# Kernel tuning notes

Measured on AMD Instinct MI355X. Metric: run time of the kernel, lower is better.

The kernel has to match this reference:

```python
import jax, jax.numpy as jnp
import numpy as np


def setup_inputs() -> dict:
    key = jax.random.key(0)
    k1, k2, k3, k4 = jax.random.split(key, 4)
    B, C, H, W = 8, 512, 64, 64  # h must equal w per the broadcast in the original
    opt = jax.random.normal(k1, (B, C, H, W), dtype=jnp.float32)
    sar = jax.random.normal(k2, (B, C, H, W), dtype=jnp.float32)
    # 1x1 conv weights, shape [out_c, in_c] (kernel spatial dims are 1x1)
    W_opt = jax.random.normal(k3, (C, C), dtype=jnp.float32) * (2.0 / C) ** 0.5
    W_sar = jax.random.normal(k4, (C, C), dtype=jnp.float32) * (2.0 / C) ** 0.5
    return {"opt": opt, "sar": sar, "W_opt": W_opt, "W_sar": W_sar}


def _branch(x, Wc):
    # 1x1 conv: per-pixel channel mixing. Q = K = V (same conv applied to same input).
    f = jnp.einsum('oc,bchw->bohw', Wc, x)            # (b,c,h,w)
    # S[b,c,i,j] = sum_h Q[b,c,h,i] * K[b,c,h,j]  (transpose(2,3) @ original)
    S = jnp.einsum('bchi,bchj->bcij', f, f)           # (b,c,w,w)
    # nn.Softmax() with no dim on 4D -> softmax over channel dim (axis=1)
    S = jax.nn.softmax(S, axis=1)
    return f, S


def reference(opt, sar, W_opt, W_sar):
    V_opt, S_opt = _branch(opt, W_opt)
    V_sar, S_sar = _branch(sar, W_sar)
    hadamard = S_opt * S_sar                          # (b,c,w,w); h==w lets it broadcast with V
    Att = (V_opt * hadamard) * (V_sar * hadamard)
    return Att
```

## Files before the change

### kernel.cpp

```cpp
#include <hip/hip_runtime.h>
#include <cstdint>

#define CCH 512
#define HW  4096
#define WDIM 64
#define NBATCH 8
#define CHW ((size_t)CCH * HW)

typedef __attribute__((ext_vector_type(8))) short bf16x8;
typedef __attribute__((ext_vector_type(4))) float f32x4;
typedef __attribute__((ext_vector_type(4))) unsigned u32x4;

__device__ __forceinline__ unsigned short f2bf(float x) {
  unsigned u = __float_as_uint(x);
  unsigned r = (u + 0x7FFFu + ((u >> 16) & 1u)) >> 16;
  return (unsigned short)r;
}
__device__ __forceinline__ float bf2f(unsigned short h) {
  return __uint_as_float(((unsigned)h) << 16);
}

__device__ __forceinline__ void gl_lds16(const void* g, void* l) {
  __builtin_amdgcn_global_load_lds(
      (const __attribute__((address_space(1))) void*)g,
      (__attribute__((address_space(3))) void*)l, 16, 0, 0);
}

__global__ __launch_bounds__(256) void wsplit_k(
    const float* __restrict__ Wo, const float* __restrict__ Wsr,
    unsigned short* __restrict__ Whl) {
  const int br = blockIdx.y;
  const float* W = br ? Wsr : Wo;
  const int i = blockIdx.x * 256 + threadIdx.x;
  const float x = W[i];
  const unsigned short h = f2bf(x);
  unsigned short* dst = Whl + (size_t)br * 524288;
  dst[i] = h;
  dst[262144 + i] = f2bf(x - bf2f(h));
}

__global__ __launch_bounds__(256, 2) void mfma_conv_k(
    const unsigned short* __restrict__ Whl,
    const float* __restrict__ opt, const float* __restrict__ sar,
    float* __restrict__ F, int b0) {
  const int z = blockIdx.z;
  const int br = z & 1, bl = z >> 1;
  const unsigned short* Ah_g = Whl + (size_t)br * 524288;
  const unsigned short* Al_g = Ah_g + 262144;
  const float* Xb = (br ? sar : opt) + (size_t)(b0 + bl) * CHW;
  const int n0 = blockIdx.x * 128, m0 = blockIdx.y * 128;

  __shared__ __align__(16) unsigned short Ahs[2][128 * 32];
  __shared__ __align__(16) unsigned short Als[2][128 * 32];
  __shared__ __align__(16) unsigned short Xhs[2][128 * 32];
  __shared__ __align__(16) unsigned short Xls[2][128 * 32];

  const int tid = threadIdx.x;
  const int wave = tid >> 6, lane = tid & 63;
  const int wm = (wave >> 1) * 64, wn = (wave & 1) * 64;

  f32x4 acc[4][4] = {};

  const int rl = lane >> 2;
  const int kcA = (((lane & 3) ^ ((lane >> 3) & 3)) * 8);

  const int rX = lane;
  const int pX = (wave ^ ((lane >> 1) & 3)) * 8;

  const int fr = lane & 15;
  const int kq = (((lane >> 4) ^ ((lane >> 1) & 3)) * 8);

  float xv[16];

  auto stageA = [&](int k0, int cb) {
#pragma unroll
    for (int q = 0; q < 2; ++q) {
      const int rbase = wave * 32 + q * 16;
      const int r = rbase + rl;
      gl_lds16(Ah_g + (size_t)(m0 + r) * CCH + k0 + kcA, &Ahs[cb][rbase * 32]);
      gl_lds16(Al_g + (size_t)(m0 + r) * CCH + k0 + kcA, &Als[cb][rbase * 32]);
    }
  };

  auto loadX = [&](int k0) {
#pragma unroll
    for (int s = 0; s < 8; ++s) {
      const size_t rowb = (size_t)(k0 + wave * 8 + s) * HW + n0;
      xv[s] = Xb[rowb + rX];
      xv[8 + s] = Xb[rowb + 64 + rX];
    }
  };

  auto writeX = [&](int cb) {
    u32x4 h0, h1, l0, l1;
#pragma unroll
    for (int w = 0; w < 4; ++w) {
      const unsigned a0 = __float_as_uint(xv[2 * w]);
      const unsigned a1 = __float_as_uint(xv[2 * w + 1]);
      const unsigned b0_ = __float_as_uint(xv[8 + 2 * w]);
      const unsigned b1_ = __float_as_uint(xv[8 + 2 * w + 1]);
      h0[w] = __builtin_amdgcn_perm(a1, a0, 0x07060302u);
      h1[w] = __builtin_amdgcn_perm(b1_, b0_, 0x07060302u);
      const float la0 = xv[2 * w] - __uint_as_float(a0 & 0xFFFF0000u);
      const float la1 = xv[2 * w + 1] - __uint_as_float(a1 & 0xFFFF0000u);
      const float lb0 = xv[8 + 2 * w] - __uint_as_float(b0_ & 0xFFFF0000u);
      const float lb1 = xv[8 + 2 * w + 1] - __uint_as_float(b1_ & 0xFFFF0000u);
      l0[w] = __builtin_amdgcn_perm(__float_as_uint(la1), __float_as_uint(la0),
                                    0x07060302u);
      l1[w] = __builtin_amdgcn_perm(__float_as_uint(lb1), __float_as_uint(lb0),
                                    0x07060302u);
    }
    *(u32x4*)&Xhs[cb][rX * 32 + pX] = h0;
    *(u32x4*)&Xhs[cb][(rX + 64) * 32 + pX] = h1;
    *(u32x4*)&Xls[cb][rX * 32 + pX] = l0;
    *(u32x4*)&Xls[cb][(rX + 64) * 32 + pX] = l1;
  };

  auto compute = [&](int cb) {
    bf16x8 bh[4], blo[4];
#pragma unroll
    for (int j = 0; j < 4; ++j) {
      const int n = wn + j * 16 + fr;
      bh[j] = *(const bf16x8*)&Xhs[cb][n * 32 + kq];
      blo[j] = *(const bf16x8*)&Xls[cb][n * 32 + kq];
    }
#pragma unroll
    for (int i = 0; i < 4; ++i) {
      const int m = wm + i * 16 + fr;
      const bf16x8 ah = *(const bf16x8*)&Ahs[cb][m * 32 + kq];
      const bf16x8 al = *(const bf16x8*)&Als[cb][m * 32 + kq];
#pragma unroll
      for (int j = 0; j < 4; ++j) {
        acc[i][j] = __builtin_amdgcn_mfma_f32_16x16x32_bf16(ah, bh[j], acc[i][j], 0, 0, 0);
        acc[i][j] = __builtin_amdgcn_mfma_f32_16x16x32_bf16(ah, blo[j], acc[i][j], 0, 0, 0);
        acc[i][j] = __builtin_amdgcn_mfma_f32_16x16x32_bf16(al, bh[j], acc[i][j], 0, 0, 0);
      }
    }
  };

  stageA(0, 0);
  loadX(0);
  writeX(0);
  __syncthreads();

  int cur = 0;
  for (int t = 0; t < 15; ++t) {
    const int k0n = (t + 1) * 32;
    stageA(k0n, cur ^ 1);
    loadX(k0n);
    compute(cur);
    writeX(cur ^ 1);
    __syncthreads();
    cur ^= 1;
  }
  compute(cur);

  float* Fb = F + (size_t)z * CHW;
  const int col = lane & 15, rq = (lane >> 4) * 4;
#pragma unroll
  for (int i = 0; i < 4; ++i)
#pragma unroll
    for (int j = 0; j < 4; ++j) {
      const int n = n0 + wn + j * 16 + col;
#pragma unroll
      for (int r = 0; r < 4; ++r) {
        const int m = m0 + wm + i * 16 + rq + r;
        Fb[(size_t)m * HW + n] = acc[i][j][r];
      }
    }
}

#define FT_S 72
__global__ __launch_bounds__(256, 4) void gram_k(
    const float* __restrict__ F, float* __restrict__ S) {
  const size_t base = ((size_t)blockIdx.y * CCH + blockIdx.x) * HW;
  const float* Fc = F + base;
  float* Sc = S + base;

  __shared__ float Fs[64 * 64];
  __shared__ unsigned short FtH[64 * FT_S];
  __shared__ unsigned short FtL[64 * FT_S];

  const int tid = threadIdx.x;
  const int wave = tid >> 6, lane = tid & 63;

#pragma unroll
  for (int t = 0; t < 4; ++t) {
    const int off = (wave * 4 + t) * 256;
    gl_lds16(Fc + off + lane * 4, &Fs[off]);
  }
  __syncthreads();

  {
    const int w = lane;
    const int hc = wave * 16;
    unsigned short hb[16], lb[16];
#pragma unroll
    for (int k = 0; k < 16; ++k) {
      const float x = Fs[(hc + k) * 64 + w];
      const unsigned short h = f2bf(x);
      hb[k] = h;
      lb[k] = f2bf(x - bf2f(h));
    }
    unsigned short* dh = &FtH[w * FT_S + hc];
    unsigned short* dl = &FtL[w * FT_S + hc];
    *(uint4*)(dh + 0) = *(uint4*)&hb[0];
    *(uint4*)(dh + 8) = *(uint4*)&hb[8];
    *(uint4*)(dl + 0) = *(uint4*)&lb[0];
    *(uint4*)(dl + 8) = *(uint4*)&lb[8];
  }
  __syncthreads();

  const int wm = (wave >> 1) * 32, wn = (wave & 1) * 32;
  const int fr = lane & 15, kq = (lane >> 4) * 8;

  f32x4 acc[2][2] = {};
#pragma unroll
  for (int kcc = 0; kcc < 2; ++kcc) {
    bf16x8 ah[2], al[2], bh[2], bl[2];
#pragma unroll
    for (int i = 0; i < 2; ++i) {
      ah[i] = *(const bf16x8*)&FtH[(wm + i * 16 + fr) * FT_S + kcc * 32 + kq];
      al[i] = *(const bf16x8*)&FtL[(wm + i * 16 + fr) * FT_S + kcc * 32 + kq];
      bh[i] = *(const bf16x8*)&FtH[(wn + i * 16 + fr) * FT_S + kcc * 32 + kq];
      bl[i] = *(const bf16x8*)&FtL[(wn + i * 16 + fr) * FT_S + kcc * 32 + kq];
    }
#pragma unroll
    for (int i = 0; i < 2; ++i)
#pragma unroll
      for (int j = 0; j < 2; ++j) {
        acc[i][j] = __builtin_amdgcn_mfma_f32_16x16x32_bf16(ah[i], bh[j], acc[i][j], 0, 0, 0);
        acc[i][j] = __builtin_amdgcn_mfma_f32_16x16x32_bf16(ah[i], bl[j], acc[i][j], 0, 0, 0);
        acc[i][j] = __builtin_amdgcn_mfma_f32_16x16x32_bf16(al[i], bh[j], acc[i][j], 0, 0, 0);
      }
  }

  const int rq = (lane >> 4) * 4;
#pragma unroll
  for (int i = 0; i < 2; ++i)
#pragma unroll
    for (int j = 0; j < 2; ++j) {
      const int n = wn + j * 16 + fr;
#pragma unroll
      for (int r = 0; r < 4; ++r) {
        const int m = wm + i * 16 + rq + r;
        Sc[m * 64 + n] = acc[i][j][r];
      }
    }
}

__global__ __launch_bounds__(1024, 4) void softmax_fuse_k(
    const float* __restrict__ S, const float* __restrict__ Fbuf,
    float* __restrict__ Out) {
  const int i = blockIdx.x;
  const int b = blockIdx.y;
  const int tid = threadIdx.x;
  const int jl = (tid & 15) * 4;
  const int g = tid >> 4;

  const size_t rowO = (size_t)(b * 2) * CHW + (size_t)i * WDIM;
  const size_t rowS = rowO + CHW;

  float4 xoc[8], xsc[8];
  float mo[4], lo[4], ms[4], ls[4];
#pragma unroll
  for (int k = 0; k < 4; ++k) { mo[k] = -1e30f; ms[k] = -1e30f; lo[k] = 0.f; ls[k] = 0.f; }

#pragma unroll
  for (int cc = 0; cc < 8; ++cc) {
    const int c = g * 8 + cc;
    const size_t off = (size_t)c * HW + jl;
    xoc[cc] = *(const float4*)&S[rowO + off];
    xsc[cc] = *(const float4*)&S[rowS + off];
    mo[0] = fmaxf(mo[0], xoc[cc].x); mo[1] = fmaxf(mo[1], xoc[cc].y);
    mo[2] = fmaxf(mo[2], xoc[cc].z); mo[3] = fmaxf(mo[3], xoc[cc].w);
    ms[0] = fmaxf(ms[0], xsc[cc].x); ms[1] = fmaxf(ms[1], xsc[cc].y);
    ms[2] = fmaxf(ms[2], xsc[cc].z); ms[3] = fmaxf(ms[3], xsc[cc].w);
  }
#pragma unroll
  for (int cc = 0; cc < 8; ++cc) {
    lo[0] += __expf(xoc[cc].x - mo[0]); lo[1] += __expf(xoc[cc].y - mo[1]);
    lo[2] += __expf(xoc[cc].z - mo[2]); lo[3] += __expf(xoc[cc].w - mo[3]);
    ls[0] += __expf(xsc[cc].x - ms[0]); ls[1] += __expf(xsc[cc].y - ms[1]);
    ls[2] += __expf(xsc[cc].z - ms[2]); ls[3] += __expf(xsc[cc].w - ms[3]);
  }

  __shared__ float sm[2][64][64];
  __shared__ float sl[2][64][64];
  __shared__ float Mf[2][64];
  __shared__ float Li[2][64];

  *(float4*)&sm[0][g][jl] = make_float4(mo[0], mo[1], mo[2], mo[3]);
  *(float4*)&sl[0][g][jl] = make_float4(lo[0], lo[1], lo[2], lo[3]);
  *(float4*)&sm[1][g][jl] = make_float4(ms[0], ms[1], ms[2], ms[3]);
  *(float4*)&sl[1][g][jl] = make_float4(ls[0], ls[1], ls[2], ls[3]);
  __syncthreads();

  if (tid < 128) {
    const int br = tid >> 6, j = tid & 63;
    float M = -1e30f;
#pragma unroll 16
    for (int t = 0; t < 64; ++t) M = fmaxf(M, sm[br][t][j]);
    float L = 0.f;
#pragma unroll 16
    for (int t = 0; t < 64; ++t) L += sl[br][t][j] * __expf(sm[br][t][j] - M);
    Mf[br][j] = M;
    Li[br][j] = 1.f / L;
  }
  __syncthreads();

  float4 Mo4 = *(const float4*)&Mf[0][jl];
  float4 iLo4 = *(const float4*)&Li[0][jl];
  float4 Ms4 = *(const float4*)&Mf[1][jl];
  float4 iLs4 = *(const float4*)&Li[1][jl];
  float Mov[4] = {Mo4.x, Mo4.y, Mo4.z, Mo4.w};
  float iLov[4] = {iLo4.x, iLo4.y, iLo4.z, iLo4.w};
  float Msv[4] = {Ms4.x, Ms4.y, Ms4.z, Ms4.w};
  float iLsv[4] = {iLs4.x, iLs4.y, iLs4.z, iLs4.w};

#pragma unroll
  for (int cc = 0; cc < 8; ++cc) {
    const int c = g * 8 + cc;
    const size_t off = (size_t)c * HW + jl;
    float4 fo = *(const float4*)&Fbuf[rowO + off];
    float4 fs = *(const float4*)&Fbuf[rowS + off];
    float xov[4] = {xoc[cc].x, xoc[cc].y, xoc[cc].z, xoc[cc].w};
    float xsv[4] = {xsc[cc].x, xsc[cc].y, xsc[cc].z, xsc[cc].w};
    float fov[4] = {fo.x, fo.y, fo.z, fo.w};
    float fsv[4] = {fs.x, fs.y, fs.z, fs.w};
    float ov[4];
#pragma unroll
    for (int k = 0; k < 4; ++k) {
      const float ho = __expf(xov[k] - Mov[k]) * iLov[k];
      const float hs = __expf(xsv[k] - Msv[k]) * iLsv[k];
      float h2 = ho * hs;
      h2 *= h2;
      ov[k] = fov[k] * fsv[k] * h2;
    }
    *(float4*)&Out[(size_t)b * CHW + (size_t)c * HW + (size_t)i * WDIM + jl] =
        make_float4(ov[0], ov[1], ov[2], ov[3]);
  }
}

extern "C" void kernel_launch(void* const* d_in, const int* in_sizes, int n_in,
                              void* d_out, int out_size, void* d_ws, size_t ws_size,
                              hipStream_t stream) {
  const float* opt = (const float*)d_in[0];
  const float* sar = (const float*)d_in[1];
  const float* Wo  = (const float*)d_in[2];
  const float* Wsr = (const float*)d_in[3];
  float* out = (float*)d_out;

  unsigned short* Whl = (unsigned short*)d_ws;
  const size_t whlElems = 2u * 2u * 262144u;
  const size_t perBl = 2 * CHW;
  const size_t perBlBytes = perBl * 8;
  int bc = (int)((ws_size - whlElems * 2) / perBlBytes);
  if (bc < 1) bc = 1;
  if (bc > NBATCH) bc = NBATCH;
  const int passes = (NBATCH + bc - 1) / bc;
  const int nbp = (NBATCH + passes - 1) / passes;

  float* Fbuf = (float*)(Whl + whlElems);
  float* Sbuf = Fbuf + (size_t)bc * perBl;

  hipLaunchKernelGGL(wsplit_k, dim3(1024, 2), dim3(256), 0, stream, Wo, Wsr, Whl);

  for (int b0 = 0; b0 < NBATCH; b0 += nbp) {
    const int nb = (NBATCH - b0 < nbp) ? (NBATCH - b0) : nbp;

    hipLaunchKernelGGL(mfma_conv_k, dim3(32, 4, nb * 2), dim3(256), 0, stream,
                       Whl, opt, sar, Fbuf, b0);

    hipLaunchKernelGGL(gram_k, dim3(CCH, nb * 2), dim3(256), 0, stream,
                       Fbuf, Sbuf);

    hipLaunchKernelGGL(softmax_fuse_k, dim3(WDIM, nb), dim3(1024), 0, stream,
                       Sbuf, Fbuf, out + (size_t)b0 * CHW);
  }
}
```

Measured before the change: 409.0 us.

## Single-buffer LDS in conv GEMM and raise occupancy to four blocks per CU

Replaces the double-buffered LDS tiles in the 1x1-conv MFMA kernel with single buffers, halving shared memory from 64KB to 32KB per block. Launch bounds rise from 2 to 4 blocks per SM so more waves can hide latency. The cost is a second barrier per K step and loss of overlap between the async A-tile staging and compute. Register pressure is also capped more tightly, which may cause spills given the 64 accumulator floats per thread.

```diff
diff --git a/kernel.cpp b/kernel.cpp
--- a/kernel.cpp
+++ b/kernel.cpp
@@ -39,7 +39,7 @@
   dst[262144 + i] = f2bf(x - bf2f(h));
 }
 
-__global__ __launch_bounds__(256, 2) void mfma_conv_k(
+__global__ __launch_bounds__(256, 4) void mfma_conv_k(
     const unsigned short* __restrict__ Whl,
     const float* __restrict__ opt, const float* __restrict__ sar,
     float* __restrict__ F, int b0) {
@@ -50,10 +50,10 @@
   const float* Xb = (br ? sar : opt) + (size_t)(b0 + bl) * CHW;
   const int n0 = blockIdx.x * 128, m0 = blockIdx.y * 128;
 
-  __shared__ __align__(16) unsigned short Ahs[2][128 * 32];
-  __shared__ __align__(16) unsigned short Als[2][128 * 32];
-  __shared__ __align__(16) unsigned short Xhs[2][128 * 32];
-  __shared__ __align__(16) unsigned short Xls[2][128 * 32];
+  __shared__ __align__(16) unsigned short Ahs[128 * 32];
+  __shared__ __align__(16) unsigned short Als[128 * 32];
+  __shared__ __align__(16) unsigned short Xhs[128 * 32];
+  __shared__ __align__(16) unsigned short Xls[128 * 32];
 
   const int tid = threadIdx.x;
   const int wave = tid >> 6, lane = tid & 63;
@@ -72,13 +72,13 @@
 
   float xv[16];
 
-  auto stageA = [&](int k0, int cb) {
+  auto stageA = [&](int k0) {
 #pragma unroll
     for (int q = 0; q < 2; ++q) {
       const int rbase = wave * 32 + q * 16;
       const int r = rbase + rl;
-      gl_lds16(Ah_g + (size_t)(m0 + r) * CCH + k0 + kcA, &Ahs[cb][rbase * 32]);
-      gl_lds16(Al_g + (size_t)(m0 + r) * CCH + k0 + kcA, &Als[cb][rbase * 32]);
+      gl_lds16(Ah_g + (size_t)(m0 + r) * CCH + k0 + kcA, &Ahs[rbase * 32]);
+      gl_lds16(Al_g + (size_t)(m0 + r) * CCH + k0 + kcA, &Als[rbase * 32]);
     }
   };
 
@@ -91,7 +91,7 @@
     }
   };
 
-  auto writeX = [&](int cb) {
+  auto writeX = [&]() {
     u32x4 h0, h1, l0, l1;
 #pragma unroll
     for (int w = 0; w < 4; ++w) {
@@ -110,25 +110,25 @@
       l1[w] = __builtin_amdgcn_perm(__float_as_uint(lb1), __float_as_uint(lb0),
                                     0x07060302u);
     }
-    *(u32x4*)&Xhs[cb][rX * 32 + pX] = h0;
-    *(u32x4*)&Xhs[cb][(rX + 64) * 32 + pX] = h1;
-    *(u32x4*)&Xls[cb][rX * 32 + pX] = l0;
-    *(u32x4*)&Xls[cb][(rX + 64) * 32 + pX] = l1;
+    *(u32x4*)&Xhs[rX * 32 + pX] = h0;
+    *(u32x4*)&Xhs[(rX + 64) * 32 + pX] = h1;
+    *(u32x4*)&Xls[rX * 32 + pX] = l0;
+    *(u32x4*)&Xls[(rX + 64) * 32 + pX] = l1;
   };
 
-  auto compute = [&](int cb) {
+  auto compute = [&]() {
     bf16x8 bh[4], blo[4];
 #pragma unroll
     for (int j = 0; j < 4; ++j) {
       const int n = wn + j * 16 + fr;
-      bh[j] = *(const bf16x8*)&Xhs[cb][n * 32 + kq];
-      blo[j] = *(const bf16x8*)&Xls[cb][n * 32 + kq];
+      bh[j] = *(const bf16x8*)&Xhs[n * 32 + kq];
+      blo[j] = *(const bf16x8*)&Xls[n * 32 + kq];
     }
 #pragma unroll
     for (int i = 0; i < 4; ++i) {
       const int m = wm + i * 16 + fr;
-      const bf16x8 ah = *(const bf16x8*)&Ahs[cb][m * 32 + kq];
-      const bf16x8 al = *(const bf16x8*)&Als[cb][m * 32 + kq];
+      const bf16x8 ah = *(const bf16x8*)&Ahs[m * 32 + kq];
+      const bf16x8 al = *(const bf16x8*)&Als[m * 32 + kq];
 #pragma unroll
       for (int j = 0; j < 4; ++j) {
         acc[i][j] = __builtin_amdgcn_mfma_f32_16x16x32_bf16(ah, bh[j], acc[i][j], 0, 0, 0);
@@ -138,22 +138,21 @@
     }
   };
 
-  stageA(0, 0);
+  stageA(0);
   loadX(0);
-  writeX(0);
-  __syncthreads();
-
-  int cur = 0;
-  for (int t = 0; t < 15; ++t) {
-    const int k0n = (t + 1) * 32;
-    stageA(k0n, cur ^ 1);
-    loadX(k0n);
-    compute(cur);
-    writeX(cur ^ 1);
+  writeX();
+  __syncthreads();
+
+  for (int t = 0; t < 16; ++t) {
+    if (t < 15) loadX((t + 1) * 32);
+    compute();
     __syncthreads();
-    cur ^= 1;
-  }
-  compute(cur);
+    if (t < 15) {
+      stageA((t + 1) * 32);
+      writeX();
+      __syncthreads();
+    }
+  }
 
   float* Fb = F + (size_t)z * CHW;
   const int col = lane & 15, rq = (lane >> 4) * 4;
```

New measurement: 339.6 us. 1.2x faster.

## Load conv weight fragments directly from global memory instead of LDS staging

Applied to the files above, without the earlier changes.

The conv kernel stops staging the split bf16 weight tiles (hi/lo) into shared memory through global_load_lds. Each wave now reads its A fragments straight from global memory (likely served from cache, since every block reuses them) inside the compute step. This halves the LDS footprint, which allows raising launch bounds to 4 blocks per CU for more occupancy. The trade-off is that global loads now sit in the MFMA loop with no prefetch, so latency may be exposed and register pressure rises under the tighter occupancy bound.

```diff
diff --git a/kernel.cpp b/kernel.cpp
--- a/kernel.cpp
+++ b/kernel.cpp
@@ -39,7 +39,7 @@
   dst[262144 + i] = f2bf(x - bf2f(h));
 }
 
-__global__ __launch_bounds__(256, 2) void mfma_conv_k(
+__global__ __launch_bounds__(256, 4) void mfma_conv_k(
     const unsigned short* __restrict__ Whl,
     const float* __restrict__ opt, const float* __restrict__ sar,
     float* __restrict__ F, int b0) {
@@ -50,8 +50,6 @@
   const float* Xb = (br ? sar : opt) + (size_t)(b0 + bl) * CHW;
   const int n0 = blockIdx.x * 128, m0 = blockIdx.y * 128;
 
-  __shared__ __align__(16) unsigned short Ahs[2][128 * 32];
-  __shared__ __align__(16) unsigned short Als[2][128 * 32];
   __shared__ __align__(16) unsigned short Xhs[2][128 * 32];
   __shared__ __align__(16) unsigned short Xls[2][128 * 32];
 
@@ -61,26 +59,18 @@
 
   f32x4 acc[4][4] = {};
 
-  const int rl = lane >> 2;
-  const int kcA = (((lane & 3) ^ ((lane >> 3) & 3)) * 8);
-
   const int rX = lane;
   const int pX = (wave ^ ((lane >> 1) & 3)) * 8;
 
   const int fr = lane & 15;
   const int kq = (((lane >> 4) ^ ((lane >> 1) & 3)) * 8);
 
+  const unsigned short* Afh =
+      Ah_g + (size_t)(m0 + wm + fr) * CCH + ((lane >> 4) * 8);
+  const unsigned short* Afl =
+      Al_g + (size_t)(m0 + wm + fr) * CCH + ((lane >> 4) * 8);
+
   float xv[16];
-
-  auto stageA = [&](int k0, int cb) {
-#pragma unroll
-    for (int q = 0; q < 2; ++q) {
-      const int rbase = wave * 32 + q * 16;
-      const int r = rbase + rl;
-      gl_lds16(Ah_g + (size_t)(m0 + r) * CCH + k0 + kcA, &Ahs[cb][rbase * 32]);
-      gl_lds16(Al_g + (size_t)(m0 + r) * CCH + k0 + kcA, &Als[cb][rbase * 32]);
-    }
-  };
 
   auto loadX = [&](int k0) {
 #pragma unroll
@@ -116,7 +106,7 @@
     *(u32x4*)&Xls[cb][(rX + 64) * 32 + pX] = l1;
   };
 
-  auto compute = [&](int cb) {
+  auto compute = [&](int cb, int k0) {
     bf16x8 bh[4], blo[4];
 #pragma unroll
     for (int j = 0; j < 4; ++j) {
@@ -126,9 +116,8 @@
     }
 #pragma unroll
     for (int i = 0; i < 4; ++i) {
-      const int m = wm + i * 16 + fr;
-      const bf16x8 ah = *(const bf16x8*)&Ahs[cb][m * 32 + kq];
-      const bf16x8 al = *(const bf16x8*)&Als[cb][m * 32 + kq];
+      const bf16x8 ah = *(const bf16x8*)(Afh + (size_t)i * (16 * CCH) + k0);
+      const bf16x8 al = *(const bf16x8*)(Afl + (size_t)i * (16 * CCH) + k0);
 #pragma unroll
       for (int j = 0; j < 4; ++j) {
         acc[i][j] = __builtin_amdgcn_mfma_f32_16x16x32_bf16(ah, bh[j], acc[i][j], 0, 0, 0);
@@ -138,22 +127,18 @@
     }
   };
 
-  stageA(0, 0);
   loadX(0);
   writeX(0);
   __syncthreads();
 
-  int cur = 0;
-  for (int t = 0; t < 15; ++t) {
-    const int k0n = (t + 1) * 32;
-    stageA(k0n, cur ^ 1);
-    loadX(k0n);
-    compute(cur);
-    writeX(cur ^ 1);
-    __syncthreads();
-    cur ^= 1;
-  }
-  compute(cur);
+  for (int t = 0; t < 16; ++t) {
+    if (t < 15) loadX((t + 1) * 32);
+    compute(t & 1, t * 32);
+    if (t < 15) {
+      writeX((t + 1) & 1);
+      __syncthreads();
+    }
+  }
 
   float* Fb = F + (size_t)z * CHW;
   const int col = lane & 15, rq = (lane >> 4) * 4;
```

After: 444.0 us. 1.09x slower.
